# Kernel tuning notes

Measured on AMD Instinct MI355X. Metric: run time of the kernel, lower is better.

The kernel has to match this reference:

```python
import jax, jax.numpy as jnp
import numpy as np

B, S, H = 2, 2048, 1024
NH = 16
HD = H // NH  # 64


def setup_inputs() -> dict:
    key = jax.random.key(0)
    ks = jax.random.split(key, 12)
    s = 1.0 / np.sqrt(H)
    return {
        "x_q": jax.random.normal(ks[0], (B, S, H), jnp.float32),
        "x_k": jax.random.normal(ks[1], (B, S, H), jnp.float32),
        "x_v": jax.random.normal(ks[2], (B, S, H), jnp.float32),
        "attention_mask": jax.random.randint(ks[3], (B, S), 0, 2, jnp.int32),
        "Wq": jax.random.normal(ks[4], (H, H), jnp.float32) * s,
        "bq": jnp.zeros((H,), jnp.float32),
        "Wk": jax.random.normal(ks[5], (H, H), jnp.float32) * s,
        "bk": jnp.zeros((H,), jnp.float32),
        "Wv": jax.random.normal(ks[6], (H, H), jnp.float32) * s,
        "bv": jnp.zeros((H,), jnp.float32),
        "Wo": jax.random.normal(ks[7], (H, H), jnp.float32) * s,
        "bo": jnp.zeros((H,), jnp.float32),
    }


def reference(x_q, x_k, x_v, attention_mask, Wq, bq, Wk, bk, Wv, bv, Wo, bo):
    b, s, h = x_q.shape
    # projections
    q = x_q @ Wq + bq
    k = x_k @ Wk + bk
    v = x_v @ Wv + bv
    # [B, NH, S, HD]
    q = q.reshape(b, s, NH, HD).transpose(0, 2, 1, 3)
    k = k.reshape(b, s, NH, HD).transpose(0, 2, 1, 3)
    v = v.reshape(b, s, NH, HD).transpose(0, 2, 1, 3)
    scores = jnp.einsum("bhqd,bhkd->bhqk", q, k) / jnp.sqrt(jnp.float32(HD))
    # key-padding mask: 1 -> keep (0 bias), else -inf; broadcast [B,1,1,S]
    bias = jnp.where(attention_mask == 1, 0.0, -jnp.inf).astype(scores.dtype)
    scores = scores + bias[:, None, None, :]
    attn = jax.nn.softmax(scores, axis=-1)
    # dropout prob = 0.0 (eval / deterministic): identity
    out = jnp.einsum("bhqk,bhkd->bhqd", attn, v)
    out = out.transpose(0, 2, 1, 3).reshape(b, s, h)
    return out @ Wo + bo
```

## Files before the change

### kernel.cpp

```cpp
#include <hip/hip_runtime.h>

#define DEVI static __device__ __forceinline__

typedef unsigned short u16;
typedef unsigned int u32;
typedef __attribute__((ext_vector_type(8))) __bf16 bf16x8;
typedef __attribute__((ext_vector_type(8))) short short8;
typedef __attribute__((ext_vector_type(4))) float f32x4;

DEVI u16 f2bf(float f) {
  union { float f; u32 u; } v; v.f = f;
  u32 r = v.u + 0x7fffu + ((v.u >> 16) & 1u);
  return (u16)(r >> 16);
}

DEVI u16 bfc(float f) {
  union { __bf16 b; u16 u; } v; v.b = (__bf16)f; return v.u;
}

DEVI void gload16(const void* g, void* l) {
  __builtin_amdgcn_global_load_lds(
      (const __attribute__((address_space(1))) void*)g,
      (__attribute__((address_space(3))) void*)l,
      16, 0, 0);
}

__global__ void k_cvt(const float* __restrict__ in, u16* __restrict__ out, int n4) {
  int i = blockIdx.x * blockDim.x + threadIdx.x;
  if (i >= n4) return;
  const float4 v = reinterpret_cast<const float4*>(in)[i];
  ushort4 o;
  o.x = f2bf(v.x); o.y = f2bf(v.y); o.z = f2bf(v.z); o.w = f2bf(v.w);
  reinterpret_cast<ushort4*>(out)[i] = o;
}

__global__ void k_maskbias(const int* __restrict__ m, float* __restrict__ bias, int n) {
  int i = blockIdx.x * blockDim.x + threadIdx.x;
  if (i < n) bias[i] = (m[i] == 1) ? 0.f : -1e30f;
}

__global__ void k_transcvt(const float* __restrict__ W, u16* __restrict__ Wt) {
  __shared__ float tl[32][33];
  const int n0 = blockIdx.x * 32, k0 = blockIdx.y * 32;
  const int tx = threadIdx.x, ty = threadIdx.y;
#pragma unroll
  for (int r = ty; r < 32; r += 8)
    tl[r][tx] = W[(size_t)(k0 + r) * 1024 + n0 + tx];
  __syncthreads();
#pragma unroll
  for (int r = ty; r < 32; r += 8)
    Wt[(size_t)(n0 + r) * 1024 + k0 + tx] = f2bf(tl[tx][r]);
}

DEVI void store1(u16* C, size_t i, float v) { C[i] = f2bf(v); }
DEVI void store1(float* C, size_t i, float v) { C[i] = v; }

template <typename OutT>
__global__ __launch_bounds__(256, 2) void k_gemm_bt(
    const u16* __restrict__ Abase, long aZ,
    const u16* __restrict__ Btbase, long bZ,
    const float* __restrict__ bias0, const float* __restrict__ bias1,
    const float* __restrict__ bias2,
    float s0, float s1, float s2,
    OutT* __restrict__ Cbase, long cZ, u16* __restrict__ Vt,
    int M, int N, int K) {
  const int z = blockIdx.z;
  const u16* A  = Abase  + (size_t)z * aZ;
  const u16* Bt = Btbase + (size_t)z * bZ;
  OutT* C = Cbase + (size_t)z * cZ;
  const float* bias = (z == 0) ? bias0 : ((z == 1) ? bias1 : bias2);
  const float scl = (z == 0) ? s0 : ((z == 1) ? s1 : s2);

  __shared__ u16 lsA[128 * 32];
  __shared__ u16 lsB[128 * 32];

  const int t = threadIdx.x;
  const int w = t >> 6, ln = t & 63;
  const int l15 = ln & 15, lhi = ln >> 4;
  const int wr = w >> 1, wc = w & 1;
  const int m0 = blockIdx.x * 128, n0 = blockIdx.y * 128;

  f32x4 acc[4][4] = {};

  for (int kt = 0; kt < K; kt += 32) {
#pragma unroll
    for (int i = 0; i < 2; ++i) {
      const int li = i * 256 + t;
      const int row = li >> 2, cb = (li & 3) << 3;
      gload16(A + (size_t)(m0 + row) * K + kt + cb,
              (char*)lsA + (i * 256 + w * 64) * 16);
      gload16(Bt + (size_t)(n0 + row) * K + kt + cb,
              (char*)lsB + (i * 256 + w * 64) * 16);
    }
    __syncthreads();

    bf16x8 af[4], bf_[4];
#pragma unroll
    for (int m = 0; m < 4; ++m)
      af[m] = *reinterpret_cast<const bf16x8*>(
          &lsA[(wr * 64 + m * 16 + l15) * 32 + lhi * 8]);
#pragma unroll
    for (int n = 0; n < 4; ++n)
      bf_[n] = *reinterpret_cast<const bf16x8*>(
          &lsB[(wc * 64 + n * 16 + l15) * 32 + lhi * 8]);
#pragma unroll
    for (int m = 0; m < 4; ++m)
#pragma unroll
      for (int n = 0; n < 4; ++n)
        acc[m][n] = __builtin_amdgcn_mfma_f32_16x16x32_bf16(af[m], bf_[n], acc[m][n], 0, 0, 0);
    __syncthreads();
  }

  if (Vt != nullptr && z == 2) {
#pragma unroll
    for (int n = 0; n < 4; ++n) {
      const int c = n0 + wc * 64 + n * 16 + l15;
      const float bv = bias[c];
#pragma unroll
      for (int m = 0; m < 4; ++m) {
        const int r = m0 + wr * 64 + m * 16 + lhi * 4;
        ushort4 s4;
#pragma unroll
        for (int j = 0; j < 4; ++j) ((u16*)&s4)[j] = f2bf(acc[m][n][j] + bv);
        *reinterpret_cast<ushort4*>(
            &Vt[((size_t)((r >> 11) * 1024 + c)) * 2048 + (r & 2047)]) = s4;
      }
    }
    return;
  }

#pragma unroll
  for (int n = 0; n < 4; ++n) {
    const int c = n0 + wc * 64 + n * 16 + l15;
    const float bv = bias[c];
#pragma unroll
    for (int m = 0; m < 4; ++m)
#pragma unroll
      for (int j = 0; j < 4; ++j) {
        const int r = m0 + wr * 64 + m * 16 + lhi * 4 + j;
        store1(C, (size_t)r * N + c, (acc[m][n][j] + bv) * scl);
      }
  }
}

__global__ __launch_bounds__(256, 2) void k_attn(
    const u16* __restrict__ Q, const u16* __restrict__ K, const u16* __restrict__ Vt,
    const float* __restrict__ MB, u16* __restrict__ O) {
  __shared__ u16 lsK[2][64][72];
  __shared__ u16 lsV[2][64][72];
  __shared__ u16 lsPt[4][32][72];

  const int t = threadIdx.x, w = t >> 6, ln = t & 63;
  const int l15 = ln & 15, lhi = ln >> 4;
  const int fid = blockIdx.x;
  const int xcd = fid & 7, slot = fid >> 3;
  const int pair = xcd * 4 + (slot >> 4);
  const int qt = slot & 15;
  const int h = pair & 15, b = pair >> 4;

  const size_t rowQ = (size_t)b * 2048 + qt * 128 + w * 32;
  const int hc = h * 64;

  const int srow = t >> 3, scol = (t & 7) << 3;
  const u16* Kg = K + ((size_t)b * 2048 + srow) * 1024 + hc + scol;
  const u16* Vg = Vt + ((size_t)(b * 1024 + hc) + srow) * 2048 + scol;

  bf16x8 qb[2][2];
#pragma unroll
  for (int mq = 0; mq < 2; ++mq)
#pragma unroll
    for (int ks = 0; ks < 2; ++ks)
      qb[mq][ks] = *reinterpret_cast<const bf16x8*>(
          &Q[(rowQ + mq * 16 + l15) * 1024 + hc + ks * 32 + lhi * 8]);

  f32x4 o[4][2] = {};
  float mrow[2] = {-1e30f, -1e30f}, lsum[2] = {0.f, 0.f};

  short8 rk0, rk1, rv0, rv1;
  rk0 = *reinterpret_cast<const short8*>(Kg);
  rk1 = *reinterpret_cast<const short8*>(Kg + 32 * 1024);
  rv0 = *reinterpret_cast<const short8*>(Vg);
  rv1 = *reinterpret_cast<const short8*>(Vg + 32 * 2048);
  *reinterpret_cast<short8*>(&lsK[0][srow][scol]) = rk0;
  *reinterpret_cast<short8*>(&lsK[0][32 + srow][scol]) = rk1;
  *reinterpret_cast<short8*>(&lsV[0][srow][scol]) = rv0;
  *reinterpret_cast<short8*>(&lsV[0][32 + srow][scol]) = rv1;
  __syncthreads();

  int cur = 0;
  for (int nt = 0; nt < 2048; nt += 64) {
    const int ntn = (nt + 64 < 2048) ? nt + 64 : 0;
    rk0 = *reinterpret_cast<const short8*>(Kg + (size_t)ntn * 1024);
    rk1 = *reinterpret_cast<const short8*>(Kg + (size_t)(ntn + 32) * 1024);
    rv0 = *reinterpret_cast<const short8*>(Vg + ntn);
    rv1 = *reinterpret_cast<const short8*>(Vg + 32 * 2048 + ntn);

    f32x4 st[4][2] = {};
    __builtin_amdgcn_s_setprio(1);
#pragma unroll
    for (int nk = 0; nk < 4; ++nk)
#pragma unroll
      for (int ks = 0; ks < 2; ++ks) {
        const bf16x8 kb = *reinterpret_cast<const bf16x8*>(
            &lsK[cur][nk * 16 + l15][ks * 32 + lhi * 8]);
        st[nk][0] = __builtin_amdgcn_mfma_f32_16x16x32_bf16(kb, qb[0][ks], st[nk][0], 0, 0, 0);
        st[nk][1] = __builtin_amdgcn_mfma_f32_16x16x32_bf16(kb, qb[1][ks], st[nk][1], 0, 0, 0);
      }
    __builtin_amdgcn_s_setprio(0);

#pragma unroll
    for (int nk = 0; nk < 4; ++nk) {
      const f32x4 bv = *reinterpret_cast<const f32x4*>(&MB[b * 2048 + nt + nk * 16 + lhi * 4]);
#pragma unroll
      for (int mq = 0; mq < 2; ++mq)
#pragma unroll
        for (int j = 0; j < 4; ++j)
          st[nk][mq][j] += bv[j];
    }

    float al[2];
#pragma unroll
    for (int mq = 0; mq < 2; ++mq) {
      float tm = st[0][mq][0];
#pragma unroll
      for (int nk = 0; nk < 4; ++nk)
#pragma unroll
        for (int j = 0; j < 4; ++j) tm = fmaxf(tm, st[nk][mq][j]);
      tm = fmaxf(tm, __shfl_xor(tm, 16, 64));
      tm = fmaxf(tm, __shfl_xor(tm, 32, 64));
      const float mn = fmaxf(mrow[mq], tm);
      al[mq] = __builtin_amdgcn_exp2f(mrow[mq] - mn);
      mrow[mq] = mn;
      float rs = 0.f;
#pragma unroll
      for (int nk = 0; nk < 4; ++nk)
#pragma unroll
        for (int j = 0; j < 4; ++j) {
          const float p = __builtin_amdgcn_exp2f(st[nk][mq][j] - mn);
          st[nk][mq][j] = p;
          rs += p;
        }
      rs += __shfl_xor(rs, 16, 64);
      rs += __shfl_xor(rs, 32, 64);
      lsum[mq] = lsum[mq] * al[mq] + rs;
    }
    if (__any((al[0] != 1.f) || (al[1] != 1.f))) {
#pragma unroll
      for (int nd = 0; nd < 4; ++nd)
#pragma unroll
        for (int mq = 0; mq < 2; ++mq)
#pragma unroll
          for (int j = 0; j < 4; ++j) o[nd][mq][j] *= al[mq];
    }

#pragma unroll
    for (int mq = 0; mq < 2; ++mq)
#pragma unroll
      for (int nk = 0; nk < 4; ++nk) {
        ushort4 pk;
        pk.x = bfc(st[nk][mq][0]); pk.y = bfc(st[nk][mq][1]);
        pk.z = bfc(st[nk][mq][2]); pk.w = bfc(st[nk][mq][3]);
        *reinterpret_cast<ushort4*>(&lsPt[w][mq * 16 + l15][nk * 16 + lhi * 4]) = pk;
      }

    __builtin_amdgcn_s_setprio(1);
#pragma unroll
    for (int ks = 0; ks < 2; ++ks) {
      bf16x8 pb[2];
#pragma unroll
      for (int mq = 0; mq < 2; ++mq)
        pb[mq] = *reinterpret_cast<const bf16x8*>(
            &lsPt[w][mq * 16 + l15][ks * 32 + lhi * 8]);
#pragma unroll
      for (int nd = 0; nd < 4; ++nd) {
        const bf16x8 vt = *reinterpret_cast<const bf16x8*>(
            &lsV[cur][nd * 16 + l15][ks * 32 + lhi * 8]);
        o[nd][0] = __builtin_amdgcn_mfma_f32_16x16x32_bf16(vt, pb[0], o[nd][0], 0, 0, 0);
        o[nd][1] = __builtin_amdgcn_mfma_f32_16x16x32_bf16(vt, pb[1], o[nd][1], 0, 0, 0);
      }
    }
    __builtin_amdgcn_s_setprio(0);

    *reinterpret_cast<short8*>(&lsK[cur ^ 1][srow][scol]) = rk0;
    *reinterpret_cast<short8*>(&lsK[cur ^ 1][32 + srow][scol]) = rk1;
    *reinterpret_cast<short8*>(&lsV[cur ^ 1][srow][scol]) = rv0;
    *reinterpret_cast<short8*>(&lsV[cur ^ 1][32 + srow][scol]) = rv1;
    __syncthreads();
    cur ^= 1;
  }

#pragma unroll
  for (int mq = 0; mq < 2; ++mq) {
    const float inv = 1.f / lsum[mq];
#pragma unroll
    for (int nd = 0; nd < 4; ++nd) {
      ushort4 s4;
      s4.x = bfc(o[nd][mq][0] * inv); s4.y = bfc(o[nd][mq][1] * inv);
      s4.z = bfc(o[nd][mq][2] * inv); s4.w = bfc(o[nd][mq][3] * inv);
      *reinterpret_cast<ushort4*>(
          &O[(rowQ + mq * 16 + l15) * 1024 + hc + nd * 16 + lhi * 4]) = s4;
    }
  }
}

extern "C" void kernel_launch(void* const* d_in, const int* in_sizes, int n_in,
                              void* d_out, int out_size, void* d_ws, size_t ws_size,
                              hipStream_t stream) {
  const float* x_q = (const float*)d_in[0];
  const float* x_k = (const float*)d_in[1];
  const float* x_v = (const float*)d_in[2];
  const int*   msk = (const int*)d_in[3];
  const float* Wq  = (const float*)d_in[4];
  const float* bq  = (const float*)d_in[5];
  const float* Wk  = (const float*)d_in[6];
  const float* bk  = (const float*)d_in[7];
  const float* Wv  = (const float*)d_in[8];
  const float* bv  = (const float*)d_in[9];
  const float* Wo  = (const float*)d_in[10];
  const float* bo  = (const float*)d_in[11];

  const size_t NTOK = 4096, H = 1024;
  u16* xbf  = (u16*)d_ws;
  u16* wt   = xbf + 3 * NTOK * H;
  u16* qkv  = wt  + 4 * H * H;
  u16* aout = qkv + 3 * NTOK * H;
  float* mb = (float*)(aout + NTOK * H);
  u16* vtb  = qkv + 2 * NTOK * H;

  k_cvt<<<dim3(4096), dim3(256), 0, stream>>>(x_q, xbf,              1048576);
  k_cvt<<<dim3(4096), dim3(256), 0, stream>>>(x_k, xbf + NTOK * H,   1048576);
  k_cvt<<<dim3(4096), dim3(256), 0, stream>>>(x_v, xbf + 2 * NTOK * H, 1048576);
  k_maskbias<<<dim3(16), dim3(256), 0, stream>>>(msk, mb, 4096);
  k_transcvt<<<dim3(32, 32), dim3(32, 8), 0, stream>>>(Wq, wt);
  k_transcvt<<<dim3(32, 32), dim3(32, 8), 0, stream>>>(Wk, wt + H * H);
  k_transcvt<<<dim3(32, 32), dim3(32, 8), 0, stream>>>(Wv, wt + 2 * H * H);
  k_transcvt<<<dim3(32, 32), dim3(32, 8), 0, stream>>>(Wo, wt + 3 * H * H);

  const float qscale = 0.125f * 1.4426950408889634f;
  k_gemm_bt<u16><<<dim3(32, 8, 3), dim3(256), 0, stream>>>(
      xbf, (long)(NTOK * H), wt, (long)(H * H), bq, bk, bv,
      qscale, 1.f, 1.f,
      qkv, (long)(NTOK * H), vtb, 4096, 1024, 1024);

  k_attn<<<dim3(512), dim3(256), 0, stream>>>(
      qkv, qkv + NTOK * H, vtb, mb, aout);

  k_gemm_bt<float><<<dim3(32, 8, 1), dim3(256), 0, stream>>>(
      aout, 0L, wt + 3 * H * H, 0L, bo, bo, bo,
      1.f, 1.f, 1.f,
      (float*)d_out, 0L, nullptr, 4096, 1024, 1024);
}
```

Before: 156.9 us.

## Halve attention query tile, single-buffer K/V, and add lazy softmax rescaling

The attention kernel now gives each wave 16 query rows instead of 32 and launches twice as many blocks (64 query rows per block). This is meant to improve occupancy and load balance. K/V shared memory drops from double to single buffering and uses an extra barrier per iteration. Online softmax now rescales only when the running max grows by more than 8 (in log2 units), which skips most rescale work. The cost is that every K/V tile is reloaded by twice as many blocks, loads overlap less with compute, and exponent values can grow up to 2^8 before a rescale.

```diff
diff --git a/kernel.cpp b/kernel.cpp
--- a/kernel.cpp
+++ b/kernel.cpp
@@ -143,51 +143,48 @@
   }
 }
 
-__global__ __launch_bounds__(256, 2) void k_attn(
+__global__ __launch_bounds__(256) void k_attn(
     const u16* __restrict__ Q, const u16* __restrict__ K, const u16* __restrict__ Vt,
     const float* __restrict__ MB, u16* __restrict__ O) {
-  __shared__ u16 lsK[2][64][72];
-  __shared__ u16 lsV[2][64][72];
-  __shared__ u16 lsPt[4][32][72];
+  __shared__ u16 lsK[64][72];
+  __shared__ u16 lsV[64][72];
+  __shared__ u16 lsPt[4][16][72];
 
   const int t = threadIdx.x, w = t >> 6, ln = t & 63;
   const int l15 = ln & 15, lhi = ln >> 4;
   const int fid = blockIdx.x;
   const int xcd = fid & 7, slot = fid >> 3;
-  const int pair = xcd * 4 + (slot >> 4);
-  const int qt = slot & 15;
+  const int pair = xcd * 4 + (slot >> 5);
+  const int qt = slot & 31;
   const int h = pair & 15, b = pair >> 4;
 
-  const size_t rowQ = (size_t)b * 2048 + qt * 128 + w * 32;
+  const size_t rowQ = (size_t)b * 2048 + qt * 64 + w * 16;
   const int hc = h * 64;
 
   const int srow = t >> 3, scol = (t & 7) << 3;
   const u16* Kg = K + ((size_t)b * 2048 + srow) * 1024 + hc + scol;
   const u16* Vg = Vt + ((size_t)(b * 1024 + hc) + srow) * 2048 + scol;
 
-  bf16x8 qb[2][2];
-#pragma unroll
-  for (int mq = 0; mq < 2; ++mq)
-#pragma unroll
-    for (int ks = 0; ks < 2; ++ks)
-      qb[mq][ks] = *reinterpret_cast<const bf16x8*>(
-          &Q[(rowQ + mq * 16 + l15) * 1024 + hc + ks * 32 + lhi * 8]);
-
-  f32x4 o[4][2] = {};
-  float mrow[2] = {-1e30f, -1e30f}, lsum[2] = {0.f, 0.f};
+  bf16x8 qb[2];
+#pragma unroll
+  for (int ks = 0; ks < 2; ++ks)
+    qb[ks] = *reinterpret_cast<const bf16x8*>(
+        &Q[(rowQ + l15) * 1024 + hc + ks * 32 + lhi * 8]);
+
+  f32x4 o[4] = {};
+  float mrow = -1e30f, lsum = 0.f;
 
   short8 rk0, rk1, rv0, rv1;
   rk0 = *reinterpret_cast<const short8*>(Kg);
   rk1 = *reinterpret_cast<const short8*>(Kg + 32 * 1024);
   rv0 = *reinterpret_cast<const short8*>(Vg);
   rv1 = *reinterpret_cast<const short8*>(Vg + 32 * 2048);
-  *reinterpret_cast<short8*>(&lsK[0][srow][scol]) = rk0;
-  *reinterpret_cast<short8*>(&lsK[0][32 + srow][scol]) = rk1;
-  *reinterpret_cast<short8*>(&lsV[0][srow][scol]) = rv0;
-  *reinterpret_cast<short8*>(&lsV[0][32 + srow][scol]) = rv1;
+  *reinterpret_cast<short8*>(&lsK[srow][scol]) = rk0;
+  *reinterpret_cast<short8*>(&lsK[32 + srow][scol]) = rk1;
+  *reinterpret_cast<short8*>(&lsV[srow][scol]) = rv0;
+  *reinterpret_cast<short8*>(&lsV[32 + srow][scol]) = rv1;
   __syncthreads();
 
-  int cur = 0;
   for (int nt = 0; nt < 2048; nt += 64) {
     const int ntn = (nt + 64 < 2048) ? nt + 64 : 0;
     rk0 = *reinterpret_cast<const short8*>(Kg + (size_t)ntn * 1024);
@@ -195,16 +192,15 @@
     rv0 = *reinterpret_cast<const short8*>(Vg + ntn);
     rv1 = *reinterpret_cast<const short8*>(Vg + 32 * 2048 + ntn);
 
-    f32x4 st[4][2] = {};
+    f32x4 st[4] = {};
     __builtin_amdgcn_s_setprio(1);
 #pragma unroll
     for (int nk = 0; nk < 4; ++nk)
 #pragma unroll
       for (int ks = 0; ks < 2; ++ks) {
         const bf16x8 kb = *reinterpret_cast<const bf16x8*>(
-            &lsK[cur][nk * 16 + l15][ks * 32 + lhi * 8]);
-        st[nk][0] = __builtin_amdgcn_mfma_f32_16x16x32_bf16(kb, qb[0][ks], st[nk][0], 0, 0, 0);
-        st[nk][1] = __builtin_amdgcn_mfma_f32_16x16x32_bf16(kb, qb[1][ks], st[nk][1], 0, 0, 0);
+            &lsK[nk * 16 + l15][ks * 32 + lhi * 8]);
+        st[nk] = __builtin_amdgcn_mfma_f32_16x16x32_bf16(kb, qb[ks], st[nk], 0, 0, 0);
       }
     __builtin_amdgcn_s_setprio(0);
 
@@ -212,94 +208,79 @@
     for (int nk = 0; nk < 4; ++nk) {
       const f32x4 bv = *reinterpret_cast<const f32x4*>(&MB[b * 2048 + nt + nk * 16 + lhi * 4]);
 #pragma unroll
-      for (int mq = 0; mq < 2; ++mq)
-#pragma unroll
-        for (int j = 0; j < 4; ++j)
-          st[nk][mq][j] += bv[j];
-    }
-
-    float al[2];
-#pragma unroll
-    for (int mq = 0; mq < 2; ++mq) {
-      float tm = st[0][mq][0];
-#pragma unroll
-      for (int nk = 0; nk < 4; ++nk)
-#pragma unroll
-        for (int j = 0; j < 4; ++j) tm = fmaxf(tm, st[nk][mq][j]);
-      tm = fmaxf(tm, __shfl_xor(tm, 16, 64));
-      tm = fmaxf(tm, __shfl_xor(tm, 32, 64));
-      const float mn = fmaxf(mrow[mq], tm);
-      al[mq] = __builtin_amdgcn_exp2f(mrow[mq] - mn);
-      mrow[mq] = mn;
-      float rs = 0.f;
-#pragma unroll
-      for (int nk = 0; nk < 4; ++nk)
-#pragma unroll
-        for (int j = 0; j < 4; ++j) {
-          const float p = __builtin_amdgcn_exp2f(st[nk][mq][j] - mn);
-          st[nk][mq][j] = p;
-          rs += p;
-        }
-      rs += __shfl_xor(rs, 16, 64);
-      rs += __shfl_xor(rs, 32, 64);
-      lsum[mq] = lsum[mq] * al[mq] + rs;
-    }
-    if (__any((al[0] != 1.f) || (al[1] != 1.f))) {
+      for (int j = 0; j < 4; ++j) st[nk][j] += bv[j];
+    }
+
+    float tm = st[0][0];
+#pragma unroll
+    for (int nk = 0; nk < 4; ++nk)
+#pragma unroll
+      for (int j = 0; j < 4; ++j) tm = fmaxf(tm, st[nk][j]);
+    tm = fmaxf(tm, __shfl_xor(tm, 16, 64));
+    tm = fmaxf(tm, __shfl_xor(tm, 32, 64));
+
+    const bool trig = tm > mrow + 8.f;
+    if (__any(trig)) {
+      const float al = trig ? __builtin_amdgcn_exp2f(mrow - tm) : 1.f;
+      if (trig) mrow = tm;
+      lsum *= al;
 #pragma unroll
       for (int nd = 0; nd < 4; ++nd)
 #pragma unroll
-        for (int mq = 0; mq < 2; ++mq)
-#pragma unroll
-          for (int j = 0; j < 4; ++j) o[nd][mq][j] *= al[mq];
-    }
-
-#pragma unroll
-    for (int mq = 0; mq < 2; ++mq)
-#pragma unroll
-      for (int nk = 0; nk < 4; ++nk) {
-        ushort4 pk;
-        pk.x = bfc(st[nk][mq][0]); pk.y = bfc(st[nk][mq][1]);
-        pk.z = bfc(st[nk][mq][2]); pk.w = bfc(st[nk][mq][3]);
-        *reinterpret_cast<ushort4*>(&lsPt[w][mq * 16 + l15][nk * 16 + lhi * 4]) = pk;
-      }
+        for (int j = 0; j < 4; ++j) o[nd][j] *= al;
+    }
+
+    float rs = 0.f;
+#pragma unroll
+    for (int nk = 0; nk < 4; ++nk)
+#pragma unroll
+      for (int j = 0; j < 4; ++j) {
+        const float p = __builtin_amdgcn_exp2f(st[nk][j] - mrow);
+        st[nk][j] = p;
+        rs += p;
+      }
+    rs += __shfl_xor(rs, 16, 64);
+    rs += __shfl_xor(rs, 32, 64);
+    lsum += rs;
+
+#pragma unroll
+    for (int nk = 0; nk < 4; ++nk) {
+      ushort4 pk;
+      pk.x = bfc(st[nk][0]); pk.y = bfc(st[nk][1]);
+      pk.z = bfc(st[nk][2]); pk.w = bfc(st[nk][3]);
+      *reinterpret_cast<ushort4*>(&lsPt[w][l15][nk * 16 + lhi * 4]) = pk;
+    }
 
     __builtin_amdgcn_s_setprio(1);
 #pragma unroll
     for (int ks = 0; ks < 2; ++ks) {
-      bf16x8 pb[2];
-#pragma unroll
-      for (int mq = 0; mq < 2; ++mq)
-        pb[mq] = *reinterpret_cast<const bf16x8*>(
-            &lsPt[w][mq * 16 + l15][ks * 32 + lhi * 8]);
+      const bf16x8 pb = *reinterpret_cast<const bf16x8*>(
+          &lsPt[w][l15][ks * 32 + lhi * 8]);
 #pragma unroll
       for (int nd = 0; nd < 4; ++nd) {
         const bf16x8 vt = *reinterpret_cast<const bf16x8*>(
-            &lsV[cur][nd * 16 + l15][ks * 32 + lhi * 8]);
-        o[nd][0] = __builtin_amdgcn_mfma_f32_16x16x32_bf16(vt, pb[0], o[nd][0], 0, 0, 0);
-        o[nd][1] = __builtin_amdgcn_mfma_f32_16x16x32_bf16(vt, pb[1], o[nd][1], 0, 0, 0);
+            &lsV[nd * 16 + l15][ks * 32 + lhi * 8]);
+        o[nd] = __builtin_amdgcn_mfma_f32_16x16x32_bf16(vt, pb, o[nd], 0, 0, 0);
       }
     }
     __builtin_amdgcn_s_setprio(0);
 
-    *reinterpret_cast<short8*>(&lsK[cur ^ 1][srow][scol]) = rk0;
-    *reinterpret_cast<short8*>(&lsK[cur ^ 1][32 + srow][scol]) = rk1;
-    *reinterpret_cast<short8*>(&lsV[cur ^ 1][srow][scol]) = rv0;
-    *reinterpret_cast<short8*>(&lsV[cur ^ 1][32 + srow][scol]) = rv1;
     __syncthreads();
-    cur ^= 1;
-  }
-
-#pragma unroll
-  for (int mq = 0; mq < 2; ++mq) {
-    const float inv = 1.f / lsum[mq];
-#pragma unroll
-    for (int nd = 0; nd < 4; ++nd) {
-      ushort4 s4;
-      s4.x = bfc(o[nd][mq][0] * inv); s4.y = bfc(o[nd][mq][1] * inv);
-      s4.z = bfc(o[nd][mq][2] * inv); s4.w = bfc(o[nd][mq][3] * inv);
-      *reinterpret_cast<ushort4*>(
-          &O[(rowQ + mq * 16 + l15) * 1024 + hc + nd * 16 + lhi * 4]) = s4;
-    }
+    *reinterpret_cast<short8*>(&lsK[srow][scol]) = rk0;
+    *reinterpret_cast<short8*>(&lsK[32 + srow][scol]) = rk1;
+    *reinterpret_cast<short8*>(&lsV[srow][scol]) = rv0;
+    *reinterpret_cast<short8*>(&lsV[32 + srow][scol]) = rv1;
+    __syncthreads();
+  }
+
+  const float inv = 1.f / lsum;
+#pragma unroll
+  for (int nd = 0; nd < 4; ++nd) {
+    ushort4 s4;
+    s4.x = bfc(o[nd][0] * inv); s4.y = bfc(o[nd][1] * inv);
+    s4.z = bfc(o[nd][2] * inv); s4.w = bfc(o[nd][3] * inv);
+    *reinterpret_cast<ushort4*>(
+        &O[(rowQ + l15) * 1024 + hc + nd * 16 + lhi * 4]) = s4;
   }
 }
 
@@ -342,7 +323,7 @@
       qscale, 1.f, 1.f,
       qkv, (long)(NTOK * H), vtb, 4096, 1024, 1024);
 
-  k_attn<<<dim3(512), dim3(256), 0, stream>>>(
+  k_attn<<<dim3(1024), dim3(256), 0, stream>>>(
       qkv, qkv + NTOK * H, vtb, mb, aout);
 
   k_gemm_bt<float><<<dim3(32, 8, 1), dim3(256), 0, stream>>>(
```

Result: slower. 166.8 us (+6.3%).
